# Kernel tuning notes

Hardware: AMD Instinct MI355X
Metric: run time of the kernel (lower is better)

The kernel has to match this reference:

```python
import jax, jax.numpy as jnp
import numpy as np

MARGIN = 0.2  # self.margin; temperature is unused in the original forward


def setup_inputs() -> dict:
    key = jax.random.key(0)
    k1, k2 = jax.random.split(key)
    B, D, NUM_CLASSES = 512, 256, 10
    features = jax.random.normal(k1, (B, D), dtype=jnp.float32)
    labels = jax.random.randint(k2, (B,), 0, NUM_CLASSES, dtype=jnp.int32)
    return {"features": features, "labels": labels}


def reference(features, labels):
    B = features.shape[0]
    sim = features @ features.T  # [B, B]

    eq = (labels[:, None] == labels[None, :])
    pos_mask = eq.astype(sim.dtype) * (1.0 - jnp.eye(B, dtype=sim.dtype))  # diag zeroed
    neg_mask = 1.0 - eq.astype(sim.dtype)

    # For anchor row i, pos j, neg k: relu(margin + sim[i,k] - sim[i,j])
    hinge = jax.nn.relu(MARGIN + sim[:, None, :] - sim[:, :, None])  # [B, Bpos, Bneg]
    loss_sum = jnp.einsum('ijk,ij,ik->', hinge, pos_mask, neg_mask)

    pos_cnt = pos_mask.sum(axis=1)  # per-row positive counts
    neg_cnt = neg_mask.sum(axis=1)
    valid = (pos_cnt > 0) & (neg_cnt > 0)
    num_valid = valid.sum().astype(sim.dtype)

    # Original bug faithfully reproduced: denominator uses the LAST row's
    # pos/neg counts (pos_sim/neg_sim leak out of the python loop).
    denom = num_valid * pos_cnt[-1] * neg_cnt[-1]
    return jnp.where(denom > 0, loss_sum / denom, jnp.zeros((), sim.dtype))
```

## Files before the change

kernel.cpp:

```cpp
#include <hip/hip_runtime.h>

#define B 512
#define D 256
#define NCLS 10
#define MARGIN 0.2f
#define THREADS 1024
#define NWAVES (THREADS / 64)
#define ROWS 2
#define NBLOCKS (B / ROWS)
#define DT 32
#define NDT (D / DT)
#define JS 36

__global__ __launch_bounds__(THREADS) void fused_loss_kernel(
    const float* __restrict__ F, const int* __restrict__ labels,
    float* __restrict__ out)
{
    __shared__ float ldsR[B * JS];
    __shared__ float fi[ROWS][D];
    __shared__ float simrow[ROWS][B];
    __shared__ int   lbl[B];
    __shared__ float pos_vals[ROWS][B];
    __shared__ float neg_vals[ROWS][B];
    __shared__ int   cnt[ROWS][2];
    __shared__ int   hist[NCLS];
    __shared__ float wred[NWAVES];
    __shared__ int   vred[NWAVES];

    const int t    = threadIdx.x;
    const int lane = t & 63;
    const int w    = t >> 6;
    const int i0   = blockIdx.x * ROWS;
    const int r    = t >> 9;
    const int j    = t & (B - 1);

    if (t < B)    lbl[t] = labels[t];
    if (t < NCLS) hist[t] = 0;
    if (t < (ROWS * D) / 4)
        ((float4*)fi)[t] = ((const float4*)(F + (size_t)i0 * D))[t];
    if (t < ROWS * 2) ((int*)cnt)[t] = 0;
    __syncthreads();

    if (t < B) atomicAdd(&hist[lbl[t]], 1);

    float acc = 0.f;
    const float4* Fv   = (const float4*)F;
    const float*  base = &ldsR[j * JS];
    const float*  fr   = fi[r];
    for (int tile = 0; tile < NDT; ++tile) {
        const int dt4 = tile * (DT / 4);
#pragma unroll
        for (int k = 0; k < (B * DT / 4) / THREADS; ++k) {
            const int g   = t + THREADS * k;
            const int row = g >> 3;
            const int m   = g & 7;
            *(float4*)&ldsR[row * JS + 4 * m] = Fv[row * (D / 4) + dt4 + m];
        }
        __syncthreads();
        const int dt = tile * DT;
#pragma unroll
        for (int e4 = 0; e4 < DT / 4; ++e4) {
            const float4 a = *(const float4*)&fr[dt + 4 * e4];
            const float4 x = *(const float4*)&base[4 * e4];
            acc = fmaf(a.x, x.x, acc);
            acc = fmaf(a.y, x.y, acc);
            acc = fmaf(a.z, x.z, acc);
            acc = fmaf(a.w, x.w, acc);
        }
        __syncthreads();
    }
    simrow[r][j] = acc;
    __syncthreads();

    {
        bool valid = false;
        if (t < B) { const int c = hist[lbl[t]]; valid = (c >= 2) && (c <= B - 1); }
        const unsigned long long mv = __ballot(valid);
        if (lane == 0) vred[w] = __popcll(mv);
    }

    const int i_r = i0 + r;
    const int li  = lbl[i_r];
    {
        const bool active = (j != i_r);
        const bool ispos  = active && (lbl[j] == li);
        const bool isneg  = active && (lbl[j] != li);
        const unsigned long long mp = __ballot(ispos);
        const unsigned long long mn = __ballot(isneg);
        int basep = 0, basen = 0;
        if (lane == 0) {
            basep = atomicAdd(&cnt[r][0], __popcll(mp));
            basen = atomicAdd(&cnt[r][1], __popcll(mn));
        }
        basep = __shfl(basep, 0, 64);
        basen = __shfl(basen, 0, 64);
        const unsigned long long below = (1ull << lane) - 1ull;
        const float sv = simrow[r][j];
        if (ispos) pos_vals[r][basep + __popcll(mp & below)] = sv;
        if (isneg) neg_vals[r][basen + __popcll(mn & below)] = sv;
    }
    __syncthreads();

    const int P = cnt[r][0], N = cnt[r][1];
    const float nv_t = (j < N) ? neg_vals[r][j] : -1e30f;
    float local = 0.f;
    for (int pi = 0; pi < P; ++pi) {
        const float v = nv_t - (pos_vals[r][pi] - MARGIN);
        local += (v > 0.f) ? v : 0.f;
    }

#pragma unroll
    for (int off = 32; off > 0; off >>= 1)
        local += __shfl_down(local, off, 64);
    if (lane == 0) wred[w] = local;
    __syncthreads();
    if (t == 0) {
        float s = 0.f;
        int   nv = 0;
#pragma unroll
        for (int k = 0; k < NWAVES; ++k) { s += wred[k]; nv += vred[k]; }
        const int   clast = hist[lbl[B - 1]];
        const float denom = (float)nv * (float)(clast - 1) * (float)(B - clast);
        atomicAdd(out, (denom > 0.f) ? s / denom : 0.f);
    }
}

extern "C" void kernel_launch(void* const* d_in, const int* in_sizes, int n_in,
                              void* d_out, int out_size, void* d_ws, size_t ws_size,
                              hipStream_t stream) {
    const float* F      = (const float*)d_in[0];
    const int*   labels = (const int*)d_in[1];
    float* out = (float*)d_out;
    (void)d_ws; (void)ws_size;

    fused_loss_kernel<<<NBLOCKS, THREADS, 0, stream>>>(F, labels, out);
}
```

Baseline: 71.55 us.

## Double-buffer feature tiles via async global-to-LDS loads with swizzled layout and split-K

Feature tiles now go straight from global memory into a double-buffered, XOR-swizzled LDS buffer through global_load_lds, so the next tile loads while the current one is computed, with explicit vmcnt waits and raw barriers. Each half of the block takes half of every tile's K range for both anchor rows, and the two partial sums are combined through shared memory. Anchor-row features are read from global memory instead of LDS. The hinge loop reads four positives at once, using sentinel padding. This brings hand-managed waitcnt and sync that depend on the exact instruction count, and more global loads for the anchor rows.

```diff
diff --git a/kernel.cpp b/kernel.cpp
--- a/kernel.cpp
+++ b/kernel.cpp
@@ -10,67 +10,91 @@
 #define NBLOCKS (B / ROWS)
 #define DT 32
 #define NDT (D / DT)
-#define JS 36
+#define TILE_FLOATS (B * DT)
 
 __global__ __launch_bounds__(THREADS) void fused_loss_kernel(
     const float* __restrict__ F, const int* __restrict__ labels,
     float* __restrict__ out)
 {
-    __shared__ float ldsR[B * JS];
-    __shared__ float fi[ROWS][D];
-    __shared__ float simrow[ROWS][B];
-    __shared__ int   lbl[B];
-    __shared__ float pos_vals[ROWS][B];
-    __shared__ float neg_vals[ROWS][B];
-    __shared__ int   cnt[ROWS][2];
-    __shared__ int   hist[NCLS];
-    __shared__ float wred[NWAVES];
-    __shared__ int   vred[NWAVES];
+    __shared__ float  buf[2][TILE_FLOATS];
+    __shared__ float2 part[2][B];
+    __shared__ float  pos_vals[ROWS][B + 4];
+    __shared__ float  neg_vals[ROWS][B];
+    __shared__ int    lbl[B];
+    __shared__ int    cnt[ROWS][2];
+    __shared__ int    hist[NCLS];
+    __shared__ float  wred[NWAVES];
+    __shared__ int    vred[NWAVES];
 
     const int t    = threadIdx.x;
     const int lane = t & 63;
     const int w    = t >> 6;
     const int i0   = blockIdx.x * ROWS;
-    const int r    = t >> 9;
+    const int h    = t >> 9;
     const int j    = t & (B - 1);
+    const int sj   = (j & 7) ^ ((j >> 3) & 7);
+    const int h4   = __builtin_amdgcn_readfirstlane(h << 2);
 
-    if (t < B)    lbl[t] = labels[t];
-    if (t < NCLS) hist[t] = 0;
-    if (t < (ROWS * D) / 4)
-        ((float4*)fi)[t] = ((const float4*)(F + (size_t)i0 * D))[t];
+    auto stage = [&](float* dstbase, int tile) {
+#pragma unroll
+        for (int k = 0; k < 4; ++k) {
+            const int p  = (w << 8) + (k << 6) + lane;
+            const int jj = p >> 3;
+            const int e4 = (p & 7) ^ (jj & 7) ^ ((jj >> 3) & 7);
+            const float* src = F + jj * D + tile * DT + (e4 << 2);
+            float* dst = dstbase + (w << 10) + (k << 8);
+            __builtin_amdgcn_global_load_lds(
+                (const __attribute__((address_space(1))) void*)src,
+                (__attribute__((address_space(3))) void*)dst, 16, 0, 0);
+        }
+    };
+
+    if (t < B)        lbl[t] = labels[t];
+    if (t < NCLS)     hist[t] = 0;
     if (t < ROWS * 2) ((int*)cnt)[t] = 0;
-    __syncthreads();
+    stage(buf[0], 0);
+
+    asm volatile("s_waitcnt lgkmcnt(0)" ::: "memory");
+    __builtin_amdgcn_s_barrier();
 
     if (t < B) atomicAdd(&hist[lbl[t]], 1);
 
-    float acc = 0.f;
-    const float4* Fv   = (const float4*)F;
-    const float*  base = &ldsR[j * JS];
-    const float*  fr   = fi[r];
+    float acc0 = 0.f, acc1 = 0.f;
+    const float* Fa0 = F + (size_t)i0 * D;
+    const float* Fa1 = Fa0 + D;
+    int cur = 0;
     for (int tile = 0; tile < NDT; ++tile) {
-        const int dt4 = tile * (DT / 4);
-#pragma unroll
-        for (int k = 0; k < (B * DT / 4) / THREADS; ++k) {
-            const int g   = t + THREADS * k;
-            const int row = g >> 3;
-            const int m   = g & 7;
-            *(float4*)&ldsR[row * JS + 4 * m] = Fv[row * (D / 4) + dt4 + m];
+        if (tile + 1 < NDT) {
+            stage(buf[cur ^ 1], tile + 1);
+            asm volatile("s_waitcnt vmcnt(4)" ::: "memory");
+        } else {
+            asm volatile("s_waitcnt vmcnt(0)" ::: "memory");
         }
-        __syncthreads();
+        __builtin_amdgcn_s_barrier();
+        __builtin_amdgcn_sched_barrier(0);
+        const float* bufc = buf[cur];
         const int dt = tile * DT;
 #pragma unroll
-        for (int e4 = 0; e4 < DT / 4; ++e4) {
-            const float4 a = *(const float4*)&fr[dt + 4 * e4];
-            const float4 x = *(const float4*)&base[4 * e4];
-            acc = fmaf(a.x, x.x, acc);
-            acc = fmaf(a.y, x.y, acc);
-            acc = fmaf(a.z, x.z, acc);
-            acc = fmaf(a.w, x.w, acc);
+        for (int k = 0; k < 4; ++k) {
+            const int e4 = h4 + k;
+            const float4 x  = *(const float4*)&bufc[(j << 5) + ((e4 ^ sj) << 2)];
+            const float4 a0 = *(const float4*)&Fa0[dt + (e4 << 2)];
+            const float4 a1 = *(const float4*)&Fa1[dt + (e4 << 2)];
+            acc0 = fmaf(a0.x, x.x, acc0); acc0 = fmaf(a0.y, x.y, acc0);
+            acc0 = fmaf(a0.z, x.z, acc0); acc0 = fmaf(a0.w, x.w, acc0);
+            acc1 = fmaf(a1.x, x.x, acc1); acc1 = fmaf(a1.y, x.y, acc1);
+            acc1 = fmaf(a1.z, x.z, acc1); acc1 = fmaf(a1.w, x.w, acc1);
         }
-        __syncthreads();
+        __builtin_amdgcn_sched_barrier(0);
+        __builtin_amdgcn_s_barrier();
+        cur ^= 1;
     }
-    simrow[r][j] = acc;
+
+    part[h][j] = make_float2(acc0, acc1);
     __syncthreads();
+    const float2 pA = part[0][j];
+    const float2 pB = part[1][j];
+    const float  sv = h ? (pA.y + pB.y) : (pA.x + pB.x);
 
     {
         bool valid = false;
@@ -79,6 +103,7 @@
         if (lane == 0) vred[w] = __popcll(mv);
     }
 
+    const int r   = h;
     const int i_r = i0 + r;
     const int li  = lbl[i_r];
     {
@@ -95,18 +120,23 @@
         basep = __shfl(basep, 0, 64);
         basen = __shfl(basen, 0, 64);
         const unsigned long long below = (1ull << lane) - 1ull;
-        const float sv = simrow[r][j];
         if (ispos) pos_vals[r][basep + __popcll(mp & below)] = sv;
         if (isneg) neg_vals[r][basen + __popcll(mn & below)] = sv;
     }
     __syncthreads();
+    const int P = cnt[r][0], N = cnt[r][1];
+    if (j < 4) pos_vals[r][P + j] = 1e30f;
+    __syncthreads();
 
-    const int P = cnt[r][0], N = cnt[r][1];
     const float nv_t = (j < N) ? neg_vals[r][j] : -1e30f;
     float local = 0.f;
-    for (int pi = 0; pi < P; ++pi) {
-        const float v = nv_t - (pos_vals[r][pi] - MARGIN);
-        local += (v > 0.f) ? v : 0.f;
+    for (int pi = 0; pi < P; pi += 4) {
+        const float4 pv = *(const float4*)&pos_vals[r][pi];
+        float v;
+        v = nv_t - (pv.x - MARGIN); local += (v > 0.f) ? v : 0.f;
+        v = nv_t - (pv.y - MARGIN); local += (v > 0.f) ? v : 0.f;
+        v = nv_t - (pv.z - MARGIN); local += (v > 0.f) ? v : 0.f;
+        v = nv_t - (pv.w - MARGIN); local += (v > 0.f) ? v : 0.f;
     }
 
 #pragma unroll
```

Result: slower. 73.89 us (+3.3%).
